# Optimization experiments

Measured on AMD Instinct MI355X. Metric: run time of the kernel, lower is better.

## Reference

```python
import jax, jax.numpy as jnp
import numpy as np

# ---- fixed hyperparameters (match init_kwargs / internal constants) ----
N_INP, N_HID = 96, 2048
DT = 0.075
GAMMA, EPSILON = 2.7, 4.7
RHO = 0.99
INPUT_SCALING = 1.0
LIF_TAU_M = 0.5
SPIKE_GAIN = 5.0
THETA_LIF, THETA_RF = 1.0, 1.0
ALPHA, BETA = 0.0, 0.0   # fixed internally (reset scaling disabled)
TAU_REF = 0.25


def setup_inputs() -> dict:
    key = jax.random.key(0)
    k_x, k_x2h, k_h2h, k_b = jax.random.split(key, 4)
    x = jax.random.normal(k_x, (32, 1024, N_INP), dtype=jnp.float32)
    # x2h = rand(n_inp, n_hid) * input_scaling
    x2h = jax.random.uniform(k_x2h, (N_INP, N_HID), dtype=jnp.float32) * INPUT_SCALING
    # h2h = 2*(2*rand - 1), then spectral-norm scaled so spectral radius = rho
    h2h = 2.0 * (2.0 * jax.random.uniform(k_h2h, (N_HID, N_HID), dtype=jnp.float32) - 1.0)
    sr = float(np.max(np.abs(np.linalg.eigvals(np.asarray(h2h, dtype=np.float64)))))
    h2h = h2h * (RHO / sr)
    # bias = (rand*2 - 1)*0.2 + 0.05
    bias = (jax.random.uniform(k_b, (N_HID,), dtype=jnp.float32) * 2.0 - 1.0) * 0.2 + 0.05
    return {"x": x, "x2h": x2h, "h2h": h2h, "bias": bias}


def reference(x, x2h, h2h, bias):
    B, T, _ = x.shape
    dt = jnp.float32(DT)
    ref_decay = jnp.exp(jnp.float32(-DT / TAU_REF))
    zeros = jnp.zeros((B, N_HID), dtype=x.dtype)
    # carry: (hy, hz, s, lif_v, ref_period, spike_counts)
    init = (zeros, zeros, zeros, zeros, zeros, zeros)

    def step(carry, xt):
        hy, hz, s, lif_v, ref_period, cnt = carry
        input_current = xt @ x2h + s @ h2h + bias          # [B, n_hid]
        lif_v = lif_v + dt * (-lif_v / LIF_TAU_M + input_current)
        lif_s = (lif_v > THETA_LIF).astype(x.dtype)
        lif_v = lif_v - lif_s * THETA_LIF
        drive = SPIKE_GAIN * lif_s
        hz = hz + dt * (drive - GAMMA * hy - EPSILON * hz)
        hy = hy + dt * hz
        s = (hy - THETA_RF - ref_period > 0).astype(x.dtype)
        hy = hy * (1.0 - s * ALPHA)
        hz = hz * (1.0 - s * BETA)
        ref_period = ref_period * ref_decay + s
        cnt = cnt + s
        return (hy, hz, s, lif_v, ref_period, cnt), None

    xt_seq = jnp.swapaxes(x, 0, 1)                          # [T, B, n_inp]
    (_, _, _, _, _, spike_counts), _ = jax.lax.scan(step, init, xt_seq)
    return spike_counts / jnp.float32(T)
```

## Files before the change

### kernel.cpp

```cpp
#include <hip/hip_runtime.h>
#include <cmath>

#define NH 2048
#define NI 96

__global__ __launch_bounds__(256) void xin_gemm(
    const float* __restrict__ A,
    const float* __restrict__ Bm,
    float* __restrict__ C)
{
    __shared__ float At[96][68];
    __shared__ float Bt[96][68];
    const int tid = threadIdx.x;
    const int rowBase = blockIdx.y * 64;
    const int colBase = blockIdx.x * 64;

    {
        const int r = tid >> 2;
        const int sub = tid & 3;
        const float4* Arow = reinterpret_cast<const float4*>(A + (size_t)(rowBase + r) * NI);
        #pragma unroll
        for (int q = 0; q < 6; ++q) {
            const int k4 = sub + 4 * q;
            float4 v = Arow[k4];
            At[k4 * 4 + 0][r] = v.x;
            At[k4 * 4 + 1][r] = v.y;
            At[k4 * 4 + 2][r] = v.z;
            At[k4 * 4 + 3][r] = v.w;
        }
    }
    {
        const int c4 = tid & 15;
        const int k0 = tid >> 4;
        #pragma unroll
        for (int g = 0; g < 6; ++g) {
            const int kk = k0 + 16 * g;
            float4 v = *reinterpret_cast<const float4*>(Bm + (size_t)kk * NH + colBase + c4 * 4);
            *reinterpret_cast<float4*>(&Bt[kk][c4 * 4]) = v;
        }
    }
    __syncthreads();

    const int ty = tid >> 4, tx = tid & 15;
    float acc[4][4] = {};
    #pragma unroll 8
    for (int kk = 0; kk < 96; ++kk) {
        float4 a = *reinterpret_cast<const float4*>(&At[kk][ty * 4]);
        float4 b = *reinterpret_cast<const float4*>(&Bt[kk][tx * 4]);
        acc[0][0] += a.x * b.x; acc[0][1] += a.x * b.y; acc[0][2] += a.x * b.z; acc[0][3] += a.x * b.w;
        acc[1][0] += a.y * b.x; acc[1][1] += a.y * b.y; acc[1][2] += a.y * b.z; acc[1][3] += a.y * b.w;
        acc[2][0] += a.z * b.x; acc[2][1] += a.z * b.y; acc[2][2] += a.z * b.z; acc[2][3] += a.z * b.w;
        acc[3][0] += a.w * b.x; acc[3][1] += a.w * b.y; acc[3][2] += a.w * b.z; acc[3][3] += a.w * b.w;
    }
    #pragma unroll
    for (int i = 0; i < 4; ++i) {
        float4 o;
        o.x = acc[i][0]; o.y = acc[i][1]; o.z = acc[i][2]; o.w = acc[i][3];
        *reinterpret_cast<float4*>(C + (size_t)(rowBase + ty * 4 + i) * NH + colBase + tx * 4) = o;
    }
}

template <int USE_XIN>
__global__ __launch_bounds__(512) void esn_seq(
    const float* __restrict__ xin,
    const float* __restrict__ x,
    const float* __restrict__ x2h,
    const float* __restrict__ h2h,
    const float* __restrict__ bias,
    float* __restrict__ out,
    int T)
{
    const int b = blockIdx.x;
    const int tid = threadIdx.x;
    const int n0 = tid * 4;
    const int wv = tid >> 6;
    const int lane = tid & 63;

    __shared__ alignas(16) int list[NH];
    __shared__ alignas(16) int wcnt[8];
    __shared__ float xt[NI];

    constexpr float DT = 0.075f;
    constexpr float TAU_M = 0.5f;
    constexpr float GGAMMA = 2.7f;
    constexpr float GEPS = 4.7f;
    constexpr float GAIN = 5.0f;
    const float ref_decay = expf(-0.075f / 0.25f);

    float lv[4] = {0.f, 0.f, 0.f, 0.f};
    float hy[4] = {0.f, 0.f, 0.f, 0.f};
    float hz[4] = {0.f, 0.f, 0.f, 0.f};
    float rf[4] = {0.f, 0.f, 0.f, 0.f};
    float cnt[4] = {0.f, 0.f, 0.f, 0.f};
    float bs[4];
    {
        const float4 b4 = *reinterpret_cast<const float4*>(&bias[n0]);
        bs[0] = b4.x; bs[1] = b4.y; bs[2] = b4.z; bs[3] = b4.w;
    }
    int nact = 0;

    if (!USE_XIN) {
        if (tid < NI) xt[tid] = x[(size_t)b * T * NI + tid];
    }
    __syncthreads();

    const unsigned long long below = (1ull << lane) - 1ull;
    const unsigned long long lo32 = 0xFFFFFFFFull;
    const unsigned long long mb = (lane >= 32) ? (below & ~lo32) : below;

    const float* __restrict__ xrow = USE_XIN ? (xin + (size_t)b * T * NH + n0) : xin;
    const int4* __restrict__ L4 = reinterpret_cast<const int4*>(list);

    float4 xi = make_float4(0.f, 0.f, 0.f, 0.f);
    if (USE_XIN) xi = *reinterpret_cast<const float4*>(xrow);

#define ISSUE(St, grp) do {                                                           \
        I##St = L4[(grp)];                                                            \
        W##St##_0 = *reinterpret_cast<const float4*>(&h2h[(size_t)I##St.x * NH + n0]); \
        W##St##_1 = *reinterpret_cast<const float4*>(&h2h[(size_t)I##St.y * NH + n0]); \
        W##St##_2 = *reinterpret_cast<const float4*>(&h2h[(size_t)I##St.z * NH + n0]); \
        W##St##_3 = *reinterpret_cast<const float4*>(&h2h[(size_t)I##St.w * NH + n0]); \
    } while (0)
#define ACC(St) do {                                                                  \
        a0[0] += W##St##_0.x; a0[1] += W##St##_0.y; a0[2] += W##St##_0.z; a0[3] += W##St##_0.w; \
        a1[0] += W##St##_1.x; a1[1] += W##St##_1.y; a1[2] += W##St##_1.z; a1[3] += W##St##_1.w; \
        a2[0] += W##St##_2.x; a2[1] += W##St##_2.y; a2[2] += W##St##_2.z; a2[3] += W##St##_2.w; \
        a3[0] += W##St##_3.x; a3[1] += W##St##_3.y; a3[2] += W##St##_3.z; a3[3] += W##St##_3.w; \
    } while (0)

    for (int t = 0; t < T; ++t) {
        float4 xi_n;
        if (USE_XIN) {
            const int tn = (t + 1 < T) ? (t + 1) : t;
            xi_n = *reinterpret_cast<const float4*>(xrow + (size_t)tn * NH);
        }

        float a0[4] = {0.f, 0.f, 0.f, 0.f};
        float a1[4] = {0.f, 0.f, 0.f, 0.f};
        float a2[4] = {0.f, 0.f, 0.f, 0.f};
        float a3[4] = {0.f, 0.f, 0.f, 0.f};

        const int n4 = nact & ~3;
        const int G = n4 >> 2;
        const int tc = nact - n4;

        int4 I0, I1, I2, I3;
        float4 W0_0, W0_1, W0_2, W0_3;
        float4 W1_0, W1_1, W1_2, W1_3;
        float4 W2_0, W2_1, W2_2, W2_3;
        float4 W3_0, W3_1, W3_2, W3_3;

        if (0 < G) ISSUE(0, 0);
        if (1 < G) ISSUE(1, 1);
        if (2 < G) ISSUE(2, 2);
        if (3 < G) ISSUE(3, 3);
        float4 tw0, tw1, tw2;
        if (tc > 0) tw0 = *reinterpret_cast<const float4*>(&h2h[(size_t)list[n4] * NH + n0]);
        if (tc > 1) tw1 = *reinterpret_cast<const float4*>(&h2h[(size_t)list[n4 + 1] * NH + n0]);
        if (tc > 2) tw2 = *reinterpret_cast<const float4*>(&h2h[(size_t)list[n4 + 2] * NH + n0]);

        int g = 0;
        for (; g + 4 <= G; g += 4) {
            const bool r0 = (g + 4 < G), r1 = (g + 5 < G), r2 = (g + 6 < G), r3 = (g + 7 < G);
            ACC(0); if (r0) ISSUE(0, g + 4);
            ACC(1); if (r1) ISSUE(1, g + 5);
            ACC(2); if (r2) ISSUE(2, g + 6);
            ACC(3); if (r3) ISSUE(3, g + 7);
        }
        if (g + 0 < G) ACC(0);
        if (g + 1 < G) ACC(1);
        if (g + 2 < G) ACC(2);
        if (tc > 0) { a0[0] += tw0.x; a0[1] += tw0.y; a0[2] += tw0.z; a0[3] += tw0.w; }
        if (tc > 1) { a0[0] += tw1.x; a0[1] += tw1.y; a0[2] += tw1.z; a0[3] += tw1.w; }
        if (tc > 2) { a0[0] += tw2.x; a0[1] += tw2.y; a0[2] += tw2.z; a0[3] += tw2.w; }

        float ic[4];
        if (USE_XIN) {
            const float xiv[4] = {xi.x, xi.y, xi.z, xi.w};
            #pragma unroll
            for (int c = 0; c < 4; ++c) {
                const float rec = (a0[c] + a1[c]) + (a2[c] + a3[c]);
                ic[c] = (xiv[c] + rec) + bs[c];
            }
            xi = xi_n;
        } else {
            float m[4] = {0.f, 0.f, 0.f, 0.f};
            for (int i = 0; i < NI; ++i) {
                const float xv = xt[i];
                const float4 w = *reinterpret_cast<const float4*>(&x2h[(size_t)i * NH + n0]);
                m[0] += xv * w.x; m[1] += xv * w.y; m[2] += xv * w.z; m[3] += xv * w.w;
            }
            #pragma unroll
            for (int c = 0; c < 4; ++c) {
                const float rec = (a0[c] + a1[c]) + (a2[c] + a3[c]);
                ic[c] = (m[c] + rec) + bs[c];
            }
        }

        float s[4];
        #pragma unroll
        for (int c = 0; c < 4; ++c) {
            lv[c] = lv[c] + DT * (-lv[c] / TAU_M + ic[c]);
            const float ls = lv[c] > 1.0f ? 1.0f : 0.0f;
            lv[c] -= ls;
            hz[c] = hz[c] + DT * ((GAIN * ls - GGAMMA * hy[c]) - GEPS * hz[c]);
            hy[c] = hy[c] + DT * hz[c];
            s[c] = ((hy[c] - 1.0f) - rf[c]) > 0.0f ? 1.0f : 0.0f;
            rf[c] = rf[c] * ref_decay + s[c];
            cnt[c] += s[c];
        }

        const unsigned long long ba = __ballot(s[0] > 0.0f);
        const unsigned long long bb = __ballot(s[1] > 0.0f);
        const unsigned long long bc = __ballot(s[2] > 0.0f);
        const unsigned long long bd = __ballot(s[3] > 0.0f);
        if (lane == 0)
            wcnt[wv] = (int)(__popcll(ba) + __popcll(bb) + __popcll(bc) + __popcll(bd));
        __syncthreads();

        const int4 c0 = *reinterpret_cast<const int4*>(&wcnt[0]);
        const int4 c1 = *reinterpret_cast<const int4*>(&wcnt[4]);
        int pre = 0;
        pre += (wv > 0) ? c0.x : 0;
        pre += (wv > 1) ? c0.y : 0;
        pre += (wv > 2) ? c0.z : 0;
        pre += (wv > 3) ? c0.w : 0;
        pre += (wv > 4) ? c1.x : 0;
        pre += (wv > 5) ? c1.y : 0;
        pre += (wv > 6) ? c1.z : 0;
        const int tot = ((c0.x + c0.y) + (c0.z + c0.w)) + ((c1.x + c1.y) + (c1.z + c1.w));

        const int gaLo = (int)__popcll(ba & lo32);
        const int gbLo = (int)__popcll(bb & lo32);
        const int gcLo = (int)__popcll(bc & lo32);
        const int gdLo = (int)__popcll(bd & lo32);
        const int g0 = gaLo + gcLo;
        const int g1 = gbLo + gdLo;
        const int g2 = (int)(__popcll(ba) + __popcll(bc)) - g0;
        const int base02 = (lane < 32) ? 0 : (g0 + g1);
        const int base13 = (lane < 32) ? g0 : ((g0 + g1) + g2);
        const int pa = (int)__popcll(ba & mb);
        const int pb = (int)__popcll(bb & mb);
        const int pc = (int)__popcll(bc & mb);
        const int pd = (int)__popcll(bd & mb);
        const int o02 = pre + base02 + pa + pc;
        const int o13 = pre + base13 + pb + pd;
        if (s[0] > 0.0f) list[o02] = n0;
        if (s[2] > 0.0f) list[o02 + (int)((ba >> lane) & 1ull)] = n0 + 2;
        if (s[1] > 0.0f) list[o13] = n0 + 1;
        if (s[3] > 0.0f) list[o13 + (int)((bb >> lane) & 1ull)] = n0 + 3;
        nact = tot;
        if (!USE_XIN) {
            if (t + 1 < T && tid < NI) xt[tid] = x[((size_t)b * T + (t + 1)) * NI + tid];
        }
        __syncthreads();
    }
#undef ISSUE
#undef ACC

    float4 o;
    o.x = cnt[0] / (float)T;
    o.y = cnt[1] / (float)T;
    o.z = cnt[2] / (float)T;
    o.w = cnt[3] / (float)T;
    *reinterpret_cast<float4*>(out + (size_t)b * NH + n0) = o;
}

extern "C" void kernel_launch(void* const* d_in, const int* in_sizes, int n_in,
                              void* d_out, int out_size, void* d_ws, size_t ws_size,
                              hipStream_t stream) {
    const float* x    = (const float*)d_in[0];
    const float* x2h  = (const float*)d_in[1];
    const float* h2h  = (const float*)d_in[2];
    const float* bias = (const float*)d_in[3];
    float* out = (float*)d_out;

    const int M = in_sizes[0] / NI;
    const int T = 1024;
    const int B = M / T;

    const size_t xin_bytes = (size_t)M * NH * sizeof(float);
    if (ws_size >= xin_bytes) {
        float* xin = (float*)d_ws;
        dim3 grid(NH / 64, M / 64);
        xin_gemm<<<grid, 256, 0, stream>>>(x, x2h, xin);
        esn_seq<1><<<B, 512, 0, stream>>>(xin, x, x2h, h2h, bias, out, T);
    } else {
        esn_seq<0><<<B, 512, 0, stream>>>(x , x, x2h, h2h, bias, out, T);
    }
}
```

Before: 1.308 ms.

## Prefetch input projections in 4-step chunks via LDS double buffer; scalarize row indices

The per-step global load of the precomputed input projection is replaced by loading four timesteps at once into registers, staging them into a double-buffered LDS array, and reading each step from LDS. This gives the global latency several steps to hide instead of one. Separately, the h2h row indices read from the shared spike list are passed through readfirstlane so the row base addresses become wave-uniform scalars. The change uses 64KB of extra LDS and assumes T is a multiple of 4; chunk loads beyond T are skipped.

```diff
diff --git a/kernel.cpp b/kernel.cpp
--- a/kernel.cpp
+++ b/kernel.cpp
@@ -79,6 +79,7 @@
     __shared__ alignas(16) int list[NH];
     __shared__ alignas(16) int wcnt[8];
     __shared__ float xt[NI];
+    __shared__ alignas(16) float xstage[2][4][NH];
 
     constexpr float DT = 0.075f;
     constexpr float TAU_M = 0.5f;
@@ -99,7 +100,21 @@
     }
     int nact = 0;
 
-    if (!USE_XIN) {
+    const float* __restrict__ xrow = USE_XIN ? (xin + (size_t)b * T * NH + n0) : xin;
+
+    float4 P0, P1, P2, P3;
+
+    if (USE_XIN) {
+        #pragma unroll
+        for (int r = 0; r < 4; ++r) {
+            float4 v = *reinterpret_cast<const float4*>(xrow + (size_t)r * NH);
+            *reinterpret_cast<float4*>(&xstage[0][r][n0]) = v;
+        }
+        P0 = *reinterpret_cast<const float4*>(xrow + (size_t)4 * NH);
+        P1 = *reinterpret_cast<const float4*>(xrow + (size_t)5 * NH);
+        P2 = *reinterpret_cast<const float4*>(xrow + (size_t)6 * NH);
+        P3 = *reinterpret_cast<const float4*>(xrow + (size_t)7 * NH);
+    } else {
         if (tid < NI) xt[tid] = x[(size_t)b * T * NI + tid];
     }
     __syncthreads();
@@ -108,18 +123,18 @@
     const unsigned long long lo32 = 0xFFFFFFFFull;
     const unsigned long long mb = (lane >= 32) ? (below & ~lo32) : below;
 
-    const float* __restrict__ xrow = USE_XIN ? (xin + (size_t)b * T * NH + n0) : xin;
     const int4* __restrict__ L4 = reinterpret_cast<const int4*>(list);
 
-    float4 xi = make_float4(0.f, 0.f, 0.f, 0.f);
-    if (USE_XIN) xi = *reinterpret_cast<const float4*>(xrow);
-
-#define ISSUE(St, grp) do {                                                           \
-        I##St = L4[(grp)];                                                            \
-        W##St##_0 = *reinterpret_cast<const float4*>(&h2h[(size_t)I##St.x * NH + n0]); \
-        W##St##_1 = *reinterpret_cast<const float4*>(&h2h[(size_t)I##St.y * NH + n0]); \
-        W##St##_2 = *reinterpret_cast<const float4*>(&h2h[(size_t)I##St.z * NH + n0]); \
-        W##St##_3 = *reinterpret_cast<const float4*>(&h2h[(size_t)I##St.w * NH + n0]); \
+#define ISSUE(St, grp) do {                                                              \
+        I##St = L4[(grp)];                                                               \
+        const float* pr0 = h2h + (size_t)__builtin_amdgcn_readfirstlane(I##St.x) * NH;   \
+        const float* pr1 = h2h + (size_t)__builtin_amdgcn_readfirstlane(I##St.y) * NH;   \
+        const float* pr2 = h2h + (size_t)__builtin_amdgcn_readfirstlane(I##St.z) * NH;   \
+        const float* pr3 = h2h + (size_t)__builtin_amdgcn_readfirstlane(I##St.w) * NH;   \
+        W##St##_0 = *reinterpret_cast<const float4*>(pr0 + n0);                          \
+        W##St##_1 = *reinterpret_cast<const float4*>(pr1 + n0);                          \
+        W##St##_2 = *reinterpret_cast<const float4*>(pr2 + n0);                          \
+        W##St##_3 = *reinterpret_cast<const float4*>(pr3 + n0);                          \
     } while (0)
 #define ACC(St) do {                                                                  \
         a0[0] += W##St##_0.x; a0[1] += W##St##_0.y; a0[2] += W##St##_0.z; a0[3] += W##St##_0.w; \
@@ -129,11 +144,8 @@
     } while (0)
 
     for (int t = 0; t < T; ++t) {
-        float4 xi_n;
-        if (USE_XIN) {
-            const int tn = (t + 1 < T) ? (t + 1) : t;
-            xi_n = *reinterpret_cast<const float4*>(xrow + (size_t)tn * NH);
-        }
+        float4 xi;
+        if (USE_XIN) xi = *reinterpret_cast<const float4*>(&xstage[(t >> 2) & 1][t & 3][n0]);
 
         float a0[4] = {0.f, 0.f, 0.f, 0.f};
         float a1[4] = {0.f, 0.f, 0.f, 0.f};
@@ -155,9 +167,18 @@
         if (2 < G) ISSUE(2, 2);
         if (3 < G) ISSUE(3, 3);
         float4 tw0, tw1, tw2;
-        if (tc > 0) tw0 = *reinterpret_cast<const float4*>(&h2h[(size_t)list[n4] * NH + n0]);
-        if (tc > 1) tw1 = *reinterpret_cast<const float4*>(&h2h[(size_t)list[n4 + 1] * NH + n0]);
-        if (tc > 2) tw2 = *reinterpret_cast<const float4*>(&h2h[(size_t)list[n4 + 2] * NH + n0]);
+        if (tc > 0) {
+            const float* p = h2h + (size_t)__builtin_amdgcn_readfirstlane(list[n4]) * NH;
+            tw0 = *reinterpret_cast<const float4*>(p + n0);
+        }
+        if (tc > 1) {
+            const float* p = h2h + (size_t)__builtin_amdgcn_readfirstlane(list[n4 + 1]) * NH;
+            tw1 = *reinterpret_cast<const float4*>(p + n0);
+        }
+        if (tc > 2) {
+            const float* p = h2h + (size_t)__builtin_amdgcn_readfirstlane(list[n4 + 2]) * NH;
+            tw2 = *reinterpret_cast<const float4*>(p + n0);
+        }
 
         int g = 0;
         for (; g + 4 <= G; g += 4) {
@@ -182,7 +203,6 @@
                 const float rec = (a0[c] + a1[c]) + (a2[c] + a3[c]);
                 ic[c] = (xiv[c] + rec) + bs[c];
             }
-            xi = xi_n;
         } else {
             float m[4] = {0.f, 0.f, 0.f, 0.f};
             for (int i = 0; i < NI; ++i) {
@@ -216,6 +236,21 @@
         const unsigned long long bd = __ballot(s[3] > 0.0f);
         if (lane == 0)
             wcnt[wv] = (int)(__popcll(ba) + __popcll(bb) + __popcll(bc) + __popcll(bd));
+
+        if (USE_XIN && ((t & 3) == 3)) {
+            const int bufW = ((t >> 2) + 1) & 1;
+            *reinterpret_cast<float4*>(&xstage[bufW][0][n0]) = P0;
+            *reinterpret_cast<float4*>(&xstage[bufW][1][n0]) = P1;
+            *reinterpret_cast<float4*>(&xstage[bufW][2][n0]) = P2;
+            *reinterpret_cast<float4*>(&xstage[bufW][3][n0]) = P3;
+            const int cNext = (t >> 2) + 2;
+            if (cNext * 4 + 3 < T) {
+                P0 = *reinterpret_cast<const float4*>(xrow + (size_t)(cNext * 4 + 0) * NH);
+                P1 = *reinterpret_cast<const float4*>(xrow + (size_t)(cNext * 4 + 1) * NH);
+                P2 = *reinterpret_cast<const float4*>(xrow + (size_t)(cNext * 4 + 2) * NH);
+                P3 = *reinterpret_cast<const float4*>(xrow + (size_t)(cNext * 4 + 3) * NH);
+            }
+        }
         __syncthreads();
 
         const int4 c0 = *reinterpret_cast<const int4*>(&wcnt[0]);
```

Result: faster. 1.122 ms (median of 2 runs) (-14.2%).
